# Kernel optimization log

Hardware: AMD Instinct MI355X
Metric: run time of the kernel (lower is better)

## Reference

```python
import jax, jax.numpy as jnp
import numpy as np

N, E, DIM, H = 50000, 800000, 64, 2
HD = H * DIM


def setup_inputs() -> dict:
    key = jax.random.key(0)
    ks = jax.random.split(key, 16)
    s = 0.05
    return {
        "x": jax.random.normal(ks[0], (N, DIM), jnp.float32),
        "edge_index": jax.random.randint(ks[1], (2, E), 0, N, jnp.int64),
        "Wq": jax.random.normal(ks[2], (DIM, HD), jnp.float32) * s,
        "bq": jax.random.normal(ks[3], (HD,), jnp.float32) * s,
        "Wk": jax.random.normal(ks[4], (DIM, HD), jnp.float32) * s,
        "bk": jax.random.normal(ks[5], (HD,), jnp.float32) * s,
        "Wv": jax.random.normal(ks[6], (DIM, HD), jnp.float32) * s,
        "bv": jax.random.normal(ks[7], (HD,), jnp.float32) * s,
        "Wskip": jax.random.normal(ks[8], (DIM, HD), jnp.float32) * s,
        "bskip": jax.random.normal(ks[9], (HD,), jnp.float32) * s,
        "Wc": jax.random.normal(ks[10], (HD, DIM), jnp.float32) * s,
        "bc": jax.random.normal(ks[11], (DIM,), jnp.float32) * s,
        "gamma": jnp.ones((DIM,), jnp.float32),
        "beta": jnp.zeros((DIM,), jnp.float32),
    }


def reference(x, edge_index, Wq, bq, Wk, bk, Wv, bv, Wskip, bskip, Wc, bc, gamma, beta):
    src, dst = edge_index[0], edge_index[1]  # messages flow src -> dst
    # TransformerConv: per-head q/k/v projections, [N, H, D]
    q = (x @ Wq + bq).reshape(N, H, DIM)
    k = (x @ Wk + bk).reshape(N, H, DIM)
    v = (x @ Wv + bv).reshape(N, H, DIM)
    scale = 1.0 / np.sqrt(DIM).astype(np.float32)
    # edge-wise attention logits: [E, H]
    alpha = jnp.einsum('ehd,ehd->eh', q[dst], k[src]) * scale
    # segment softmax over incoming edges of each dst node (PyG softmax)
    amax = jax.ops.segment_max(alpha, dst, num_segments=N)
    a = jnp.exp(alpha - amax[dst])
    asum = jax.ops.segment_sum(a, dst, num_segments=N)
    a = a / (asum[dst] + 1e-16)
    # weighted scatter-aggregate of values: [N, H, D] -> concat heads
    out = jax.ops.segment_sum(a[:, :, None] * v[src], dst, num_segments=N)
    out = out.reshape(N, HD)
    # root/skip connection (root_weight=True default)
    out = out + (x @ Wskip + bskip)
    # concat linear: H*D -> dim
    out = out @ Wc + bc
    # pyg.LayerNorm default mode='graph': normalize over ALL nodes+features
    out = out - out.mean()
    out = out / (out.std() + 1e-5)  # std with unbiased=False (jnp default ddof=0)
    return out * gamma + beta
```

## Files before the change

kernel.cpp:

```cpp
#include <hip/hip_runtime.h>
#include <hip/hip_bf16.h>

#define N_NODES 50000
#define N_EDGES 800000
#define DIM 64
#define NHEAD 2
#define HD 128
#define NCOL 448
#define MAXDEG 64

#define NBIN 196
#define BCAP 6144
#define ACH 4096
#define ABLK 196

#define PREP_B 112
#define PROJ_B 782

typedef short bf16x8 __attribute__((ext_vector_type(8)));
typedef float f32x16 __attribute__((ext_vector_type(16)));
typedef float f32x2 __attribute__((ext_vector_type(2)));

__device__ __forceinline__ unsigned short f2bf(float f) {
    unsigned u = __float_as_uint(f);
    unsigned r = (u + 0x7fffu + ((u >> 16) & 1u)) >> 16;
    return (unsigned short)r;
}
__device__ __forceinline__ unsigned char f2fp8(float f) {
    int r = __builtin_amdgcn_cvt_pk_fp8_f32(f, f, 0, false);
    return (unsigned char)(r & 0xff);
}

__global__ __launch_bounds__(256) void k_prep(
    const float* __restrict__ Wq, const float* __restrict__ bq,
    const float* __restrict__ Wk, const float* __restrict__ bk,
    const float* __restrict__ Wv, const float* __restrict__ bv,
    const float* __restrict__ Wskip, const float* __restrict__ bskip,
    const float* __restrict__ Wc, const float* __restrict__ bc,
    unsigned short* __restrict__ WallT, float* __restrict__ ball,
    int* __restrict__ bincnt, double* __restrict__ stats)
{
    int gid = blockIdx.x * 256 + threadIdx.x;
    if (gid == 0) { stats[0] = 0.0; stats[1] = 0.0; }
    if (gid < NBIN) bincnt[gid] = 0;
    const int j = gid >> 6;
    const int d = gid & 63;
    float w, bb;
    if (j < 128) {
        w = Wq[d * HD + j] * 0.125f;
        bb = bq[j] * 0.125f;
    } else if (j < 256) {
        int jj = j - 128;
        w = Wk[d * HD + jj];
        bb = bk[jj];
    } else if (j < 384) {
        int jj = j - 256;
        int h = jj >> 6, jc = jj & 63;
        float s = 0.f, sb = 0.f;
        for (int c = 0; c < 64; c++) {
            float wc = Wc[(h * 64 + c) * DIM + jc];
            s  += Wv[d * HD + h * 64 + c] * wc;
            sb += bv[h * 64 + c] * wc;
        }
        w = s; bb = sb;
    } else {
        int jj = j - 384;
        float s = 0.f, sb = bc[jj];
        for (int c = 0; c < HD; c++) {
            float wc = Wc[c * DIM + jj];
            s  += Wskip[d * HD + c] * wc;
            sb += bskip[c] * wc;
        }
        w = s; bb = sb;
    }
    WallT[gid] = f2bf(w);
    if (d == 0) ball[j] = bb;
}

__global__ __launch_bounds__(256) void k_bin(
    const int* __restrict__ ei, int* __restrict__ bincnt,
    unsigned* __restrict__ bins)
{
    __shared__ unsigned pk[ACH];
    __shared__ unsigned char bbn[ACH];
    __shared__ unsigned ord[ACH];
    __shared__ int hist[256];
    __shared__ int lofs[256];
    __shared__ int gbase[256];
    const int t = threadIdx.x;
    const int e0 = blockIdx.x * ACH;
    for (int i = t; i < 256; i += 256) hist[i] = 0;
    __syncthreads();
    for (int i = t; i < ACH; i += 256) {
        int e = e0 + i;
        if (e < N_EDGES) {
            int src = ei[e];
            int d = ei[N_EDGES + e];
            int bin = d >> 8;
            pk[i] = (unsigned)(((d & 255) << 16) | src);
            bbn[i] = (unsigned char)bin;
            atomicAdd(&hist[bin], 1);
        } else {
            bbn[i] = 255;
        }
    }
    __syncthreads();
    int h = hist[t];
    lofs[t] = h;
    __syncthreads();
    for (int off = 1; off < 256; off <<= 1) {
        int add = (t >= off) ? lofs[t - off] : 0;
        __syncthreads();
        lofs[t] += add;
        __syncthreads();
    }
    int excl = lofs[t] - h;
    if (t < NBIN && h > 0) gbase[t] = atomicAdd(&bincnt[t], h);
    __syncthreads();
    lofs[t] = excl;
    hist[t] = 0;
    __syncthreads();
    for (int i = t; i < ACH; i += 256) {
        int bin = bbn[i];
        if (bin != 255) {
            int sl = atomicAdd(&hist[bin], 1);
            ord[lofs[bin] + sl] = pk[i];
        }
    }
    __syncthreads();
    const int w = t >> 6, lane = t & 63;
    for (int bin = w; bin < NBIN; bin += 4) {
        int cnt = hist[bin];
        int lo = lofs[bin];
        int gb = gbase[bin];
        for (int i = lane; i < cnt; i += 64) {
            int pos = gb + i;
            if (pos < BCAP) bins[(size_t)bin * BCAP + pos] = ord[lo + i];
        }
    }
}

__global__ __launch_bounds__(256) void k_ep(
    const float* __restrict__ x,
    const unsigned short* __restrict__ WallT, const float* __restrict__ ball,
    float* __restrict__ q, unsigned char* __restrict__ kv, float* __restrict__ skipc,
    const int* __restrict__ bincnt, const unsigned* __restrict__ bins,
    int* __restrict__ deg, int* __restrict__ elist)
{
    const int blk = blockIdx.x;
    const int t = threadIdx.x;
    if (blk >= PROJ_B) {
        const int bin = blk - PROJ_B;
        __shared__ int nodecnt[256];
        nodecnt[t] = 0;
        __syncthreads();
        int cnt = bincnt[bin]; if (cnt > BCAP) cnt = BCAP;
        const unsigned* bp = bins + (size_t)bin * BCAP;
        for (int i = t; i < cnt; i += 256) {
            unsigned p = bp[i];
            int local = p >> 16;
            int src = p & 0xffff;
            int sl = atomicAdd(&nodecnt[local], 1);
            if (sl < MAXDEG)
                elist[((size_t)((bin << 8) | local)) * MAXDEG + sl] = src;
        }
        __syncthreads();
        int node = (bin << 8) + t;
        if (node < N_NODES) {
            int dgv = nodecnt[t];
            deg[node] = dgv > MAXDEG ? MAXDEG : dgv;
        }
        return;
    }
    const int w = t >> 6;
    const int lane = t & 63;
    const int col = lane & 31;
    const int khalf = lane >> 5;
    const int n0 = blk * 64 + (w >> 1) * 32;
    const int ct0 = (w & 1) * 7;
    const int rowbase = 4 * khalf;

    int nread = n0 + col; if (nread >= N_NODES) nread = N_NODES - 1;
    const float* ap = x + (size_t)nread * 64 + khalf * 8;
    bf16x8 afrag[4];
#pragma unroll
    for (int kk = 0; kk < 4; kk++) {
        float4 xa = *((const float4*)(ap + kk * 16));
        float4 xb4 = *((const float4*)(ap + kk * 16 + 4));
        bf16x8 f;
        f[0] = (short)f2bf(xa.x); f[1] = (short)f2bf(xa.y);
        f[2] = (short)f2bf(xa.z); f[3] = (short)f2bf(xa.w);
        f[4] = (short)f2bf(xb4.x); f[5] = (short)f2bf(xb4.y);
        f[6] = (short)f2bf(xb4.z); f[7] = (short)f2bf(xb4.w);
        afrag[kk] = f;
    }

    for (int tt = 0; tt < 7; tt++) {
        const int gc = (ct0 + tt) * 32 + col;
        const float b = ball[gc];
        f32x16 acc;
#pragma unroll
        for (int r = 0; r < 16; r++) acc[r] = b;
        const unsigned short* bp = WallT + (size_t)gc * 64 + khalf * 8;
#pragma unroll
        for (int kk = 0; kk < 4; kk++) {
            bf16x8 bfrag = *((const bf16x8*)(bp + kk * 16));
            acc = __builtin_amdgcn_mfma_f32_32x32x16_bf16(afrag[kk], bfrag, acc, 0, 0, 0);
        }
        if (gc < 128) {
#pragma unroll
            for (int r = 0; r < 16; r++) {
                int node = n0 + (r & 3) + 8 * (r >> 2) + rowbase;
                if (node < N_NODES) q[(size_t)node * HD + gc] = acc[r];
            }
        } else if (gc < 384) {
            int ch = gc - 128;
#pragma unroll
            for (int r = 0; r < 16; r++) {
                int node = n0 + (r & 3) + 8 * (r >> 2) + rowbase;
                if (node < N_NODES) kv[(size_t)node * 256 + ch] = f2fp8(acc[r]);
            }
        } else {
#pragma unroll
            for (int r = 0; r < 16; r++) {
                int node = n0 + (r & 3) + 8 * (r >> 2) + rowbase;
                if (node < N_NODES) skipc[(size_t)node * DIM + (gc - 384)] = acc[r];
            }
        }
    }
}

__global__ __launch_bounds__(256) void k_attn(
    const float* __restrict__ q, const unsigned char* __restrict__ kv,
    const float* __restrict__ skipc,
    const int* __restrict__ deg, const int* __restrict__ elist,
    float* __restrict__ out, float* __restrict__ parts)
{
    const int w = threadIdx.x >> 6;
    const int lane = threadIdx.x & 63;
    const int g = lane >> 3;
    const int j = lane & 7;
    const int n = blockIdx.x * 4 + w;
    const float4* qp = (const float4*)(q + (size_t)n * HD);
    const float4 qa = qp[2 * j],      qb = qp[2 * j + 1];
    const float4 qc = qp[16 + 2 * j], qd = qp[17 + 2 * j];
    float acc0[8], acc1[8];
#pragma unroll
    for (int i = 0; i < 8; i++) { acc0[i] = 0.f; acc1[i] = 0.f; }
    float l0 = 0.f, l1 = 0.f;
    const int start = n * MAXDEG;
    int dg = deg[n]; if (dg > MAXDEG) dg = MAXDEG;
    const int end = start + dg;
    for (int b0 = start; b0 < end; b0 += 8) {
        int idx = b0 + g;
        bool valid = idx < end;
        int s = elist[valid ? idx : start];
        const uint2* kp = (const uint2*)(kv + (size_t)s * 256);
        uint2 K0 = kp[j], K1 = kp[8 + j];
        uint2 V0 = kp[16 + j], V1 = kp[24 + j];
        f32x2 k0a = __builtin_amdgcn_cvt_pk_f32_fp8(K0.x, false);
        f32x2 k0b = __builtin_amdgcn_cvt_pk_f32_fp8(K0.x, true);
        f32x2 k0c = __builtin_amdgcn_cvt_pk_f32_fp8(K0.y, false);
        f32x2 k0d = __builtin_amdgcn_cvt_pk_f32_fp8(K0.y, true);
        f32x2 k1a = __builtin_amdgcn_cvt_pk_f32_fp8(K1.x, false);
        f32x2 k1b = __builtin_amdgcn_cvt_pk_f32_fp8(K1.x, true);
        f32x2 k1c = __builtin_amdgcn_cvt_pk_f32_fp8(K1.y, false);
        f32x2 k1d = __builtin_amdgcn_cvt_pk_f32_fp8(K1.y, true);
        float p0 = qa.x * k0a[0] + qa.y * k0a[1] + qa.z * k0b[0] + qa.w * k0b[1]
                 + qb.x * k0c[0] + qb.y * k0c[1] + qb.z * k0d[0] + qb.w * k0d[1];
        float p1 = qc.x * k1a[0] + qc.y * k1a[1] + qc.z * k1b[0] + qc.w * k1b[1]
                 + qd.x * k1c[0] + qd.y * k1c[1] + qd.z * k1d[0] + qd.w * k1d[1];
#pragma unroll
        for (int off = 1; off < 8; off <<= 1) {
            p0 += __shfl_xor(p0, off, 64);
            p1 += __shfl_xor(p1, off, 64);
        }
        float w0 = valid ? __expf(p0) : 0.f;
        float w1 = valid ? __expf(p1) : 0.f;
        l0 += w0; l1 += w1;
        f32x2 v0a = __builtin_amdgcn_cvt_pk_f32_fp8(V0.x, false);
        f32x2 v0b = __builtin_amdgcn_cvt_pk_f32_fp8(V0.x, true);
        f32x2 v0c = __builtin_amdgcn_cvt_pk_f32_fp8(V0.y, false);
        f32x2 v0d = __builtin_amdgcn_cvt_pk_f32_fp8(V0.y, true);
        f32x2 v1a = __builtin_amdgcn_cvt_pk_f32_fp8(V1.x, false);
        f32x2 v1b = __builtin_amdgcn_cvt_pk_f32_fp8(V1.x, true);
        f32x2 v1c = __builtin_amdgcn_cvt_pk_f32_fp8(V1.y, false);
        f32x2 v1d = __builtin_amdgcn_cvt_pk_f32_fp8(V1.y, true);
        acc0[0] += w0 * v0a[0]; acc0[1] += w0 * v0a[1];
        acc0[2] += w0 * v0b[0]; acc0[3] += w0 * v0b[1];
        acc0[4] += w0 * v0c[0]; acc0[5] += w0 * v0c[1];
        acc0[6] += w0 * v0d[0]; acc0[7] += w0 * v0d[1];
        acc1[0] += w1 * v1a[0]; acc1[1] += w1 * v1a[1];
        acc1[2] += w1 * v1b[0]; acc1[3] += w1 * v1b[1];
        acc1[4] += w1 * v1c[0]; acc1[5] += w1 * v1c[1];
        acc1[6] += w1 * v1d[0]; acc1[7] += w1 * v1d[1];
    }
#pragma unroll
    for (int off = 8; off < 64; off <<= 1) {
        l0 += __shfl_xor(l0, off, 64);
        l1 += __shfl_xor(l1, off, 64);
#pragma unroll
        for (int i = 0; i < 8; i++) {
            acc0[i] += __shfl_xor(acc0[i], off, 64);
            acc1[i] += __shfl_xor(acc1[i], off, 64);
        }
    }
    if (g == 0) {
        float inv0 = 1.f / (l0 + 1e-16f), inv1 = 1.f / (l1 + 1e-16f);
        const float4* sk = (const float4*)(skipc + (size_t)n * DIM);
        float4 sa = sk[2 * j], sb = sk[2 * j + 1];
        float o[8];
        o[0] = acc0[0] * inv0 + acc1[0] * inv1 + sa.x;
        o[1] = acc0[1] * inv0 + acc1[1] * inv1 + sa.y;
        o[2] = acc0[2] * inv0 + acc1[2] * inv1 + sa.z;
        o[3] = acc0[3] * inv0 + acc1[3] * inv1 + sa.w;
        o[4] = acc0[4] * inv0 + acc1[4] * inv1 + sb.x;
        o[5] = acc0[5] * inv0 + acc1[5] * inv1 + sb.y;
        o[6] = acc0[6] * inv0 + acc1[6] * inv1 + sb.z;
        o[7] = acc0[7] * inv0 + acc1[7] * inv1 + sb.w;
        float4 r0 = {o[0], o[1], o[2], o[3]}, r1 = {o[4], o[5], o[6], o[7]};
        float4* op = (float4*)(out + (size_t)n * DIM);
        op[2 * j] = r0; op[2 * j + 1] = r1;
        float s_ = 0.f, ss = 0.f;
#pragma unroll
        for (int i = 0; i < 8; i++) { s_ += o[i]; ss += o[i] * o[i]; }
#pragma unroll
        for (int off = 1; off < 8; off <<= 1) {
            s_ += __shfl_xor(s_, off, 64);
            ss += __shfl_xor(ss, off, 64);
        }
        if (j == 0) { parts[n * 2 + 0] = s_; parts[n * 2 + 1] = ss; }
    }
}

#define RED_BLOCKS 100
__global__ __launch_bounds__(256) void k_reduce(
    const float* __restrict__ parts, double* __restrict__ stats)
{
    double s = 0.0, ss = 0.0;
    for (int i = blockIdx.x * 256 + threadIdx.x; i < N_NODES; i += RED_BLOCKS * 256) {
        s  += (double)parts[i * 2 + 0];
        ss += (double)parts[i * 2 + 1];
    }
#pragma unroll
    for (int off = 32; off > 0; off >>= 1) {
        s  += __shfl_down(s, off);
        ss += __shfl_down(ss, off);
    }
    __shared__ double sdd[8];
    int wave = threadIdx.x >> 6;
    if ((threadIdx.x & 63) == 0) { sdd[wave * 2] = s; sdd[wave * 2 + 1] = ss; }
    __syncthreads();
    if (threadIdx.x == 0) {
        double S = 0.0, SS = 0.0;
        for (int w = 0; w < 4; w++) { S += sdd[w * 2]; SS += sdd[w * 2 + 1]; }
        atomicAdd(&stats[0], S);
        atomicAdd(&stats[1], SS);
    }
}

__global__ __launch_bounds__(256) void k_norm(
    float* __restrict__ out, const double* __restrict__ stats,
    const float* __restrict__ gamma, const float* __restrict__ beta)
{
    int i = blockIdx.x * 256 + threadIdx.x;
    if (i >= N_NODES * DIM / 4) return;
    const double cnt = (double)N_NODES * (double)DIM;
    double mean = stats[0] / cnt;
    double var  = stats[1] / cnt - mean * mean;
    if (var < 0.0) var = 0.0;
    float mf = (float)mean;
    float inv = 1.0f / ((float)sqrt(var) + 1e-5f);
    float4 v = ((const float4*)out)[i];
    float4 gv = ((const float4*)gamma)[i & 15];
    float4 bv2 = ((const float4*)beta)[i & 15];
    v.x = (v.x - mf) * inv * gv.x + bv2.x;
    v.y = (v.y - mf) * inv * gv.y + bv2.y;
    v.z = (v.z - mf) * inv * gv.z + bv2.z;
    v.w = (v.w - mf) * inv * gv.w + bv2.w;
    ((float4*)out)[i] = v;
}

extern "C" void kernel_launch(void* const* d_in, const int* in_sizes, int n_in,
                              void* d_out, int out_size, void* d_ws, size_t ws_size,
                              hipStream_t stream) {
    const float* x     = (const float*)d_in[0];
    const int*   ei    = (const int*)d_in[1];
    const float* Wq    = (const float*)d_in[2];
    const float* bq    = (const float*)d_in[3];
    const float* Wk    = (const float*)d_in[4];
    const float* bk    = (const float*)d_in[5];
    const float* Wv    = (const float*)d_in[6];
    const float* bv    = (const float*)d_in[7];
    const float* Wsk   = (const float*)d_in[8];
    const float* bsk   = (const float*)d_in[9];
    const float* Wc    = (const float*)d_in[10];
    const float* bc    = (const float*)d_in[11];
    const float* gamma = (const float*)d_in[12];
    const float* beta  = (const float*)d_in[13];
    float* out = (float*)d_out;

    float* ws = (float*)d_ws;
    const size_t NF = (size_t)N_NODES * HD;
    float* q = ws;
    unsigned char* kv = (unsigned char*)(ws + NF);
    float* skipc = (float*)(kv + (size_t)N_NODES * 256);
    unsigned short* WallT = (unsigned short*)(skipc + (size_t)N_NODES * DIM);
    float* ball   = (float*)(WallT + NCOL * 64);
    int* bincnt   = (int*)(ball + NCOL);
    unsigned* bins = (unsigned*)(bincnt + 256);
    int* deg      = (int*)(bins + (size_t)NBIN * BCAP);
    int* elist    = deg + N_NODES;
    float* parts  = (float*)(elist + (size_t)N_NODES * MAXDEG);
    double* stats = (double*)(parts + (size_t)N_NODES * 2);

    hipLaunchKernelGGL(k_prep, dim3(PREP_B), dim3(256), 0, stream,
                       Wq, bq, Wk, bk, Wv, bv, Wsk, bsk, Wc, bc,
                       WallT, ball, bincnt, stats);
    hipLaunchKernelGGL(k_bin, dim3(ABLK), dim3(256), 0, stream, ei, bincnt, bins);
    hipLaunchKernelGGL(k_ep, dim3(PROJ_B + NBIN), dim3(256), 0, stream,
                       x, WallT, ball, q, kv, skipc, bincnt, bins, deg, elist);
    hipLaunchKernelGGL(k_attn, dim3(N_NODES / 4), dim3(256), 0, stream,
                       q, kv, skipc, deg, elist, out, parts);
    hipLaunchKernelGGL(k_reduce, dim3(RED_BLOCKS), dim3(256), 0, stream, parts, stats);
    hipLaunchKernelGGL(k_norm, dim3(N_NODES * DIM / 4 / 256 + 1), dim3(256), 0, stream,
                       out, stats, gamma, beta);
}
```

Baseline: 192.3 us.

## Merge weight prep and edge binning into one launch, prefetch edge list via shuffles

```diff
diff --git a/kernel.cpp b/kernel.cpp
--- a/kernel.cpp
+++ b/kernel.cpp
@@ -11,8 +11,8 @@
 
 #define NBIN 196
 #define BCAP 6144
-#define ACH 4096
-#define ABLK 196
+#define ACH 2048
+#define BIN_BLKS 391
 
 #define PREP_B 112
 #define PROJ_B 782
@@ -31,65 +31,63 @@
     return (unsigned char)(r & 0xff);
 }
 
-__global__ __launch_bounds__(256) void k_prep(
+__global__ __launch_bounds__(256) void k_pb(
+    const int* __restrict__ ei,
     const float* __restrict__ Wq, const float* __restrict__ bq,
     const float* __restrict__ Wk, const float* __restrict__ bk,
     const float* __restrict__ Wv, const float* __restrict__ bv,
     const float* __restrict__ Wskip, const float* __restrict__ bskip,
     const float* __restrict__ Wc, const float* __restrict__ bc,
     unsigned short* __restrict__ WallT, float* __restrict__ ball,
-    int* __restrict__ bincnt, double* __restrict__ stats)
+    int* __restrict__ bincnt, unsigned* __restrict__ bins,
+    double* __restrict__ stats)
 {
-    int gid = blockIdx.x * 256 + threadIdx.x;
-    if (gid == 0) { stats[0] = 0.0; stats[1] = 0.0; }
-    if (gid < NBIN) bincnt[gid] = 0;
-    const int j = gid >> 6;
-    const int d = gid & 63;
-    float w, bb;
-    if (j < 128) {
-        w = Wq[d * HD + j] * 0.125f;
-        bb = bq[j] * 0.125f;
-    } else if (j < 256) {
-        int jj = j - 128;
-        w = Wk[d * HD + jj];
-        bb = bk[jj];
-    } else if (j < 384) {
-        int jj = j - 256;
-        int h = jj >> 6, jc = jj & 63;
-        float s = 0.f, sb = 0.f;
-        for (int c = 0; c < 64; c++) {
-            float wc = Wc[(h * 64 + c) * DIM + jc];
-            s  += Wv[d * HD + h * 64 + c] * wc;
-            sb += bv[h * 64 + c] * wc;
-        }
-        w = s; bb = sb;
-    } else {
-        int jj = j - 384;
-        float s = 0.f, sb = bc[jj];
-        for (int c = 0; c < HD; c++) {
-            float wc = Wc[c * DIM + jj];
-            s  += Wskip[d * HD + c] * wc;
-            sb += bskip[c] * wc;
-        }
-        w = s; bb = sb;
-    }
-    WallT[gid] = f2bf(w);
-    if (d == 0) ball[j] = bb;
-}
-
-__global__ __launch_bounds__(256) void k_bin(
-    const int* __restrict__ ei, int* __restrict__ bincnt,
-    unsigned* __restrict__ bins)
-{
+    const int t = threadIdx.x;
+    if (blockIdx.x < PREP_B) {
+        int gid = blockIdx.x * 256 + t;
+        if (gid == 0) { stats[0] = 0.0; stats[1] = 0.0; }
+        const int j = gid >> 6;
+        const int d = gid & 63;
+        float w, bb;
+        if (j < 128) {
+            w = Wq[d * HD + j] * 0.125f;
+            bb = bq[j] * 0.125f;
+        } else if (j < 256) {
+            int jj = j - 128;
+            w = Wk[d * HD + jj];
+            bb = bk[jj];
+        } else if (j < 384) {
+            int jj = j - 256;
+            int h = jj >> 6, jc = jj & 63;
+            float s = 0.f, sb = 0.f;
+            for (int c = 0; c < 64; c++) {
+                float wc = Wc[(h * 64 + c) * DIM + jc];
+                s  += Wv[d * HD + h * 64 + c] * wc;
+                sb += bv[h * 64 + c] * wc;
+            }
+            w = s; bb = sb;
+        } else {
+            int jj = j - 384;
+            float s = 0.f, sb = bc[jj];
+            for (int c = 0; c < HD; c++) {
+                float wc = Wc[c * DIM + jj];
+                s  += Wskip[d * HD + c] * wc;
+                sb += bskip[c] * wc;
+            }
+            w = s; bb = sb;
+        }
+        WallT[gid] = f2bf(w);
+        if (d == 0) ball[j] = bb;
+        return;
+    }
     __shared__ unsigned pk[ACH];
     __shared__ unsigned char bbn[ACH];
     __shared__ unsigned ord[ACH];
     __shared__ int hist[256];
     __shared__ int lofs[256];
     __shared__ int gbase[256];
-    const int t = threadIdx.x;
-    const int e0 = blockIdx.x * ACH;
-    for (int i = t; i < 256; i += 256) hist[i] = 0;
+    const int e0 = (blockIdx.x - PREP_B) * ACH;
+    hist[t] = 0;
     __syncthreads();
     for (int i = t; i < ACH; i += 256) {
         int e = e0 + i;
@@ -244,17 +242,16 @@
     const float4* qp = (const float4*)(q + (size_t)n * HD);
     const float4 qa = qp[2 * j],      qb = qp[2 * j + 1];
     const float4 qc = qp[16 + 2 * j], qd = qp[17 + 2 * j];
+    const int myE = elist[(size_t)n * MAXDEG + lane];
     float acc0[8], acc1[8];
 #pragma unroll
     for (int i = 0; i < 8; i++) { acc0[i] = 0.f; acc1[i] = 0.f; }
     float l0 = 0.f, l1 = 0.f;
-    const int start = n * MAXDEG;
     int dg = deg[n]; if (dg > MAXDEG) dg = MAXDEG;
-    const int end = start + dg;
-    for (int b0 = start; b0 < end; b0 += 8) {
+    for (int b0 = 0; b0 < dg; b0 += 8) {
         int idx = b0 + g;
-        bool valid = idx < end;
-        int s = elist[valid ? idx : start];
+        bool valid = idx < dg;
+        int s = __shfl(myE, valid ? idx : 0, 64);
         const uint2* kp = (const uint2*)(kv + (size_t)s * 256);
         uint2 K0 = kp[j], K1 = kp[8 + j];
         uint2 V0 = kp[16 + j], V1 = kp[24 + j];
@@ -414,10 +411,10 @@
     float* parts  = (float*)(elist + (size_t)N_NODES * MAXDEG);
     double* stats = (double*)(parts + (size_t)N_NODES * 2);
 
-    hipLaunchKernelGGL(k_prep, dim3(PREP_B), dim3(256), 0, stream,
-                       Wq, bq, Wk, bk, Wv, bv, Wsk, bsk, Wc, bc,
-                       WallT, ball, bincnt, stats);
-    hipLaunchKernelGGL(k_bin, dim3(ABLK), dim3(256), 0, stream, ei, bincnt, bins);
+    hipMemsetAsync(bincnt, 0, NBIN * sizeof(int), stream);
+    hipLaunchKernelGGL(k_pb, dim3(PREP_B + BIN_BLKS), dim3(256), 0, stream,
+                       ei, Wq, bq, Wk, bk, Wv, bv, Wsk, bsk, Wc, bc,
+                       WallT, ball, bincnt, bins, stats);
     hipLaunchKernelGGL(k_ep, dim3(PROJ_B + NBIN), dim3(256), 0, stream,
                        x, WallT, ball, q, kv, skipc, bincnt, bins, deg, elist);
     hipLaunchKernelGGL(k_attn, dim3(N_NODES / 4), dim3(256), 0, stream,
```

Measured after the change: 188.4 us. -2.0%, faster.
